# Kernel tuning notes

Hardware: AMD Instinct MI355X
Metric: run time of the kernel (lower is better)

## Reference

```python
import jax, jax.numpy as jnp
import numpy as np

HEAD_COUNT = 8  # matches init_kwargs head_count

def _branch(q_in, k_in, v_in, Wq, bq, Wk, bk, Wv, bv):
    # q_in/k_in/v_in: [B, N, D]. Linear (efficient) attention, per-head.
    B, N, D = q_in.shape
    H = HEAD_COUNT
    hd = D // H
    q = q_in @ Wq + bq            # [B, N, D]
    k = k_in @ Wk + bk
    v = v_in @ Wv + bv
    # permute(0,2,1) then contiguous channel slices per head == [B,H,hd,N]
    q = q.reshape(B, N, H, hd).transpose(0, 2, 3, 1)  # [B,H,hd,Nq]
    k = k.reshape(B, N, H, hd).transpose(0, 2, 3, 1)  # [B,H,hd,Nk]
    v = v.reshape(B, N, H, hd).transpose(0, 2, 3, 1)  # [B,H,hd,Nk]
    q = jax.nn.softmax(q, axis=3)  # softmax over sequence positions (torch dim=2)
    k = jax.nn.softmax(k, axis=2)  # softmax over head channels (torch dim=1)
    # context = k @ v^T : [B,H,hd_c,hd_d]
    ctx = jnp.einsum('bhcn,bhdn->bhcd', k, v)
    # attended = context^T @ q : [B,H,hd_d,Nq]
    att = jnp.einsum('bhcd,bhcn->bhdn', ctx, q)
    # concat heads along channel dim, then transpose -> [B, Nq, D]
    return att.reshape(B, D, N).transpose(0, 2, 1)

def setup_inputs() -> dict:
    key = jax.random.key(0)
    ks = jax.random.split(key, 16)
    B, N, D = 4, 8192, 256
    s = 0.02
    inp = {
        'f1': jax.random.normal(ks[0], (B, N, D), jnp.float32),
        'f2': jax.random.normal(ks[1], (B, N, D), jnp.float32),
        'f3': jax.random.normal(ks[2], (B, N, D), jnp.float32),
        'f4': jax.random.normal(ks[3], (B, N, D), jnp.float32),
        'f1_pos_embed': jax.random.normal(ks[4], (B, N, D), jnp.float32),
        'f2_pos_embed': jax.random.normal(ks[5], (B, N, D), jnp.float32),
        'f3_pos_embed': jax.random.normal(ks[6], (B, N, D), jnp.float32),
        'f4_pos_embed': jax.random.normal(ks[7], (B, N, D), jnp.float32),
        'Wq': jax.random.normal(ks[8], (3, D, D), jnp.float32) * s,
        'bq': jax.random.normal(ks[9], (3, D), jnp.float32) * s,
        'Wk': jax.random.normal(ks[10], (3, D, D), jnp.float32) * s,
        'bk': jax.random.normal(ks[11], (3, D), jnp.float32) * s,
        'Wv': jax.random.normal(ks[12], (3, D, D), jnp.float32) * s,
        'bv': jax.random.normal(ks[13], (3, D), jnp.float32) * s,
        'Wrp': jax.random.normal(ks[14], (3 * D, D), jnp.float32) * s,
        'brp': jax.random.normal(ks[15], (D,), jnp.float32) * s,
    }
    return inp

def reference(f1, f2, f3, f4, f1_pos_embed, f2_pos_embed, f3_pos_embed, f4_pos_embed,
              Wq, bq, Wk, bk, Wv, bv, Wrp, brp):
    q_in = f1 + f1_pos_embed
    agg21 = _branch(q_in, f2 + f2_pos_embed, f2, Wq[0], bq[0], Wk[0], bk[0], Wv[0], bv[0])
    agg31 = _branch(q_in, f3 + f3_pos_embed, f3, Wq[1], bq[1], Wk[1], bk[1], Wv[1], bv[1])
    agg41 = _branch(q_in, f4 + f4_pos_embed, f4, Wq[2], bq[2], Wk[2], bk[2], Wv[2], bv[2])
    out = jnp.concatenate([agg21, agg31, agg41], axis=-1)  # [B, N, 3D]
    return out @ Wrp + brp  # dropout p=0.0 -> identity
```

## Files before the change

kernel.cpp:

```cpp
#include <hip/hip_runtime.h>
#include <hip/hip_bf16.h>

typedef __attribute__((ext_vector_type(8))) short short8;
typedef __attribute__((ext_vector_type(4))) short shortx4;
typedef __attribute__((ext_vector_type(4))) float floatx4;
typedef __attribute__((ext_vector_type(16))) float floatx16;

#define N_SEQ 8192
#define M_ROWS 32768

__device__ __forceinline__ unsigned short f2bf(float f) {
    unsigned int x = __builtin_bit_cast(unsigned int, f);
    x += 0x7fff + ((x >> 16) & 1);
    return (unsigned short)(x >> 16);
}

__global__ __launch_bounds__(256) void transpose_w(
    const float* __restrict__ Wq, const float* __restrict__ Wk,
    const float* __restrict__ Wv, unsigned short* __restrict__ Wt)
{
    int job = blockIdx.x;
    int k = blockIdx.y;
    int n = threadIdx.x;
    const float* src =
        (job < 3) ? (Wq + job * 65536) :
        (job < 6) ? (Wk + (job - 3) * 65536) :
                    (Wv + (job - 6) * 65536);
    Wt[(size_t)job * 65536 + n * 256 + k] = f2bf(src[k * 256 + n]);
}

__global__ __launch_bounds__(256) void projq_kernel(
    const float* __restrict__ f1, const float* __restrict__ p1,
    const float* __restrict__ bq, const unsigned short* __restrict__ Wt,
    unsigned short* __restrict__ expQ, float* __restrict__ S)
{
    __shared__ __align__(16) unsigned short As[64][264];
    int m0 = blockIdx.x * 64;
    int b = m0 >> 13;
    int tid = threadIdx.x;
    int lane = tid & 63, wave = tid >> 6;
    int wm = wave >> 1, wn = wave & 1;
    int quad = lane >> 4, l15 = lane & 15;

    {
        int row = tid >> 2, seg = tid & 3;
        const float* fr = f1 + (size_t)(m0 + row) * 256 + seg * 64;
        const float* pr = p1 + (size_t)(m0 + row) * 256 + seg * 64;
        #pragma unroll
        for (int q = 0; q < 8; q++) {
            float4 x0 = *(const float4*)(fr + q * 8);
            float4 x1 = *(const float4*)(fr + q * 8 + 4);
            float4 y0 = *(const float4*)(pr + q * 8);
            float4 y1 = *(const float4*)(pr + q * 8 + 4);
            short8 v;
            v[0] = (short)f2bf(x0.x + y0.x); v[1] = (short)f2bf(x0.y + y0.y);
            v[2] = (short)f2bf(x0.z + y0.z); v[3] = (short)f2bf(x0.w + y0.w);
            v[4] = (short)f2bf(x1.x + y1.x); v[5] = (short)f2bf(x1.y + y1.y);
            v[6] = (short)f2bf(x1.z + y1.z); v[7] = (short)f2bf(x1.w + y1.w);
            *(short8*)&As[row][seg * 64 + q * 8] = v;
        }
    }
    __syncthreads();

    for (int nj = 0; nj < 6; nj++) {
        int j = nj >> 1;
        int n0 = (nj & 1) * 128;
        const unsigned short* Wj = Wt + (size_t)j * 65536;

        floatx4 acc[2][4];
        #pragma unroll
        for (int sm = 0; sm < 2; sm++)
            #pragma unroll
            for (int sn = 0; sn < 4; sn++)
                #pragma unroll
                for (int r = 0; r < 4; r++) acc[sm][sn][r] = 0.0f;

        #pragma unroll
        for (int ks = 0; ks < 8; ks++) {
            short8 af[2], bfr[4];
            #pragma unroll
            for (int sm = 0; sm < 2; sm++)
                af[sm] = *(const short8*)&As[wm * 32 + sm * 16 + l15][ks * 32 + quad * 8];
            #pragma unroll
            for (int sn = 0; sn < 4; sn++) {
                int ncol = n0 + wn * 64 + sn * 16 + l15;
                bfr[sn] = *(const short8*)(Wj + (size_t)ncol * 256 + ks * 32 + quad * 8);
            }
            #pragma unroll
            for (int sm = 0; sm < 2; sm++)
                #pragma unroll
                for (int sn = 0; sn < 4; sn++)
                    acc[sm][sn] = __builtin_amdgcn_mfma_f32_16x16x32_bf16(
                        af[sm], bfr[sn], acc[sm][sn], 0, 0, 0);
        }

        float colsum[4] = {0.f, 0.f, 0.f, 0.f};
        #pragma unroll
        for (int sm = 0; sm < 2; sm++)
            #pragma unroll
            for (int sn = 0; sn < 4; sn++) {
                float bb = bq[j * 256 + n0 + wn * 64 + sn * 16 + l15];
                #pragma unroll
                for (int r = 0; r < 4; r++) {
                    float e = __expf(acc[sm][sn][r] + bb);
                    colsum[sn] += e;
                    int row = m0 + wm * 32 + sm * 16 + quad * 4 + r;
                    int col = j * 256 + n0 + wn * 64 + sn * 16 + l15;
                    expQ[(size_t)row * 768 + col] = f2bf(e);
                }
            }
        #pragma unroll
        for (int sn = 0; sn < 4; sn++) {
            float v = colsum[sn];
            v += __shfl_xor(v, 16, 64);
            v += __shfl_xor(v, 32, 64);
            if (quad == 0)
                atomicAdd(&S[b * 768 + j * 256 + n0 + wn * 64 + sn * 16 + l15], v);
        }
    }
}

__global__ __launch_bounds__(512, 4) void projkv_ctx(
    const float* __restrict__ f2, const float* __restrict__ f3, const float* __restrict__ f4,
    const float* __restrict__ p2, const float* __restrict__ p3, const float* __restrict__ p4,
    const float* __restrict__ bk, const float* __restrict__ bv,
    const unsigned short* __restrict__ Wt, float* __restrict__ ctx)
{
    __shared__ __align__(16) unsigned short sh[36864];

    int tid = threadIdx.x;
    int lane = tid & 63, wn = tid >> 6;
    int quad = lane >> 4, l15 = lane & 15;
    int srow = tid >> 3, seg = tid & 7;

    int gbase = -1;
    int cur_ib = -1;
    const float *fin = nullptr, *pin = nullptr;
    const unsigned short *Wk_ = nullptr, *Wv_ = nullptr;
    float bkk[2] = {0.f, 0.f}, bvv[2] = {0.f, 0.f};
    floatx16 ctxacc;

    for (int j = 0; j < 3; j++) {
        int tau = blockIdx.x * 3 + j;
        int ib = tau >> 7;
        if (ib != cur_ib) {
            if (gbase >= 0) {
                int d = lane & 31;
                #pragma unroll
                for (int reg = 0; reg < 16; reg++) {
                    int cc = (reg & 3) + 8 * (reg >> 2) + 4 * (lane >> 5);
                    atomicAdd(&ctx[(size_t)gbase * 1024 + cc * 32 + d], ctxacc[reg]);
                }
            }
            cur_ib = ib;
            int b = ib & 3, i = ib >> 2;
            fin = ((i == 0) ? f2 : (i == 1) ? f3 : f4) + (size_t)b * N_SEQ * 256;
            pin = ((i == 0) ? p2 : (i == 1) ? p3 : p4) + (size_t)b * N_SEQ * 256;
            Wk_ = Wt + (size_t)(3 + i) * 65536;
            Wv_ = Wt + (size_t)(6 + i) * 65536;
            #pragma unroll
            for (int sn = 0; sn < 2; sn++) {
                bkk[sn] = bk[i * 256 + wn * 32 + sn * 16 + l15];
                bvv[sn] = bv[i * 256 + wn * 32 + sn * 16 + l15];
            }
            gbase = i * 32 + b * 8 + wn;
            #pragma unroll
            for (int q = 0; q < 16; q++) ctxacc[q] = 0.0f;
        }
        int m0 = (tau & 127) * 64;

        __syncthreads();
        {
            const float* fr = fin + (size_t)(m0 + srow) * 256;
            const float* pr = pin + (size_t)(m0 + srow) * 256;
            #pragma unroll
            for (int q = 0; q < 4; q++) {
                int c0 = q * 64 + seg * 8;
                float4 x0 = *(const float4*)(fr + c0);
                float4 x1 = *(const float4*)(fr + c0 + 4);
                float4 y0 = *(const float4*)(pr + c0);
                float4 y1 = *(const float4*)(pr + c0 + 4);
                short8 vv, kk;
                vv[0] = (short)f2bf(x0.x); kk[0] = (short)f2bf(x0.x + y0.x);
                vv[1] = (short)f2bf(x0.y); kk[1] = (short)f2bf(x0.y + y0.y);
                vv[2] = (short)f2bf(x0.z); kk[2] = (short)f2bf(x0.z + y0.z);
                vv[3] = (short)f2bf(x0.w); kk[3] = (short)f2bf(x0.w + y0.w);
                vv[4] = (short)f2bf(x1.x); kk[4] = (short)f2bf(x1.x + y1.x);
                vv[5] = (short)f2bf(x1.y); kk[5] = (short)f2bf(x1.y + y1.y);
                vv[6] = (short)f2bf(x1.z); kk[6] = (short)f2bf(x1.z + y1.z);
                vv[7] = (short)f2bf(x1.w); kk[7] = (short)f2bf(x1.w + y1.w);
                *(short8*)&sh[srow * 264 + c0] = kk;
                *(short8*)&sh[18432 + srow * 264 + c0] = vv;
            }
        }
        __syncthreads();

        floatx4 acc[4][2];
        #pragma unroll
        for (int sm = 0; sm < 4; sm++)
            #pragma unroll
            for (int sn = 0; sn < 2; sn++)
                #pragma unroll
                for (int r = 0; r < 4; r++) acc[sm][sn][r] = 0.0f;
        #pragma unroll
        for (int ks = 0; ks < 8; ks++) {
            short8 af[4], bfr[2];
            #pragma unroll
            for (int sm = 0; sm < 4; sm++)
                af[sm] = *(const short8*)&sh[(sm * 16 + l15) * 264 + ks * 32 + quad * 8];
            #pragma unroll
            for (int sn = 0; sn < 2; sn++) {
                int ncol = wn * 32 + sn * 16 + l15;
                bfr[sn] = *(const short8*)(Wk_ + (size_t)ncol * 256 + ks * 32 + quad * 8);
            }
            #pragma unroll
            for (int sm = 0; sm < 4; sm++)
                #pragma unroll
                for (int sn = 0; sn < 2; sn++)
                    acc[sm][sn] = __builtin_amdgcn_mfma_f32_16x16x32_bf16(
                        af[sm], bfr[sn], acc[sm][sn], 0, 0, 0);
        }
        #pragma unroll
        for (int sm = 0; sm < 4; sm++)
            #pragma unroll
            for (int r = 0; r < 4; r++) {
                float e0 = __expf(acc[sm][0][r] + bkk[0]);
                float e1 = __expf(acc[sm][1][r] + bkk[1]);
                float t = e0 + e1;
                t += __shfl_xor(t, 1, 64);
                t += __shfl_xor(t, 2, 64);
                t += __shfl_xor(t, 4, 64);
                t += __shfl_xor(t, 8, 64);
                float inv = 1.0f / t;
                acc[sm][0][r] = e0 * inv;
                acc[sm][1][r] = e1 * inv;
            }
        __syncthreads();
        #pragma unroll
        for (int sm = 0; sm < 4; sm++)
            #pragma unroll
            for (int sn = 0; sn < 2; sn++) {
                shortx4 v;
                #pragma unroll
                for (int r = 0; r < 4; r++) v[r] = (short)f2bf(acc[sm][sn][r]);
                *(shortx4*)&sh[(wn * 32 + sn * 16 + l15) * 72 + sm * 16 + quad * 4] = v;
            }

        #pragma unroll
        for (int sm = 0; sm < 4; sm++)
            #pragma unroll
            for (int sn = 0; sn < 2; sn++)
                #pragma unroll
                for (int r = 0; r < 4; r++) acc[sm][sn][r] = 0.0f;
        #pragma unroll
        for (int ks = 0; ks < 8; ks++) {
            short8 af[4], bfr[2];
            #pragma unroll
            for (int sm = 0; sm < 4; sm++)
                af[sm] = *(const short8*)&sh[18432 + (sm * 16 + l15) * 264 + ks * 32 + quad * 8];
            #pragma unroll
            for (int sn = 0; sn < 2; sn++) {
                int ncol = wn * 32 + sn * 16 + l15;
                bfr[sn] = *(const short8*)(Wv_ + (size_t)ncol * 256 + ks * 32 + quad * 8);
            }
            #pragma unroll
            for (int sm = 0; sm < 4; sm++)
                #pragma unroll
                for (int sn = 0; sn < 2; sn++)
                    acc[sm][sn] = __builtin_amdgcn_mfma_f32_16x16x32_bf16(
                        af[sm], bfr[sn], acc[sm][sn], 0, 0, 0);
        }
        __syncthreads();
        #pragma unroll
        for (int sm = 0; sm < 4; sm++)
            #pragma unroll
            for (int sn = 0; sn < 2; sn++) {
                shortx4 v;
                #pragma unroll
                for (int r = 0; r < 4; r++) v[r] = (short)f2bf(acc[sm][sn][r] + bvv[sn]);
                *(shortx4*)&sh[18432 + (wn * 32 + sn * 16 + l15) * 72 + sm * 16 + quad * 4] = v;
            }

        {
            int hc = wn * 32 + (lane & 31);
            int nb = (lane >> 5) * 8;
            #pragma unroll
            for (int s = 0; s < 4; s++) {
                short8 afr  = *(const short8*)&sh[hc * 72 + s * 16 + nb];
                short8 bfr2 = *(const short8*)&sh[18432 + hc * 72 + s * 16 + nb];
                ctxacc = __builtin_amdgcn_mfma_f32_32x32x16_bf16(afr, bfr2, ctxacc, 0, 0, 0);
            }
        }
    }

    if (gbase >= 0) {
        int d = lane & 31;
        #pragma unroll
        for (int reg = 0; reg < 16; reg++) {
            int cc = (reg & 3) + 8 * (reg >> 2) + 4 * (lane >> 5);
            atomicAdd(&ctx[(size_t)gbase * 1024 + cc * 32 + d], ctxacc[reg]);
        }
    }
}

__global__ __launch_bounds__(256) void wtilde_kernel(
    const float* __restrict__ ctx, const float* __restrict__ S,
    const float* __restrict__ Wrp, unsigned short* __restrict__ Wtld)
{
    __shared__ float cp[1024];
    int g = blockIdx.x;
    int i = g >> 5, b = (g >> 3) & 3, h = g & 7;
    int t = threadIdx.x;
    #pragma unroll
    for (int q = 0; q < 4; q++) {
        int idx = t + q * 256;
        int c = idx >> 5;
        cp[idx] = ctx[(size_t)g * 1024 + idx] / S[b * 768 + i * 256 + h * 32 + c];
    }
    __syncthreads();
    float accv[32];
    #pragma unroll
    for (int c = 0; c < 32; c++) accv[c] = 0.0f;
    for (int d = 0; d < 32; d++) {
        float w = Wrp[(size_t)(i * 256 + h * 32 + d) * 256 + t];
        #pragma unroll
        for (int c = 0; c < 32; c++) accv[c] += cp[c * 32 + d] * w;
    }
    for (int c = 0; c < 32; c++)
        Wtld[((size_t)b * 256 + t) * 768 + i * 256 + h * 32 + c] = f2bf(accv[c]);
}

__global__ __launch_bounds__(256) void out_kernel(
    const unsigned short* __restrict__ expQ, const unsigned short* __restrict__ Wtld,
    const float* __restrict__ brp, float* __restrict__ outp)
{
    __shared__ __align__(16) unsigned short As[128][72];
    int m0 = blockIdx.x * 128;
    int n0 = blockIdx.y * 128;
    int b = m0 >> 13;
    const unsigned short* Wb = Wtld + (size_t)b * 256 * 768;
    int tid = threadIdx.x;
    int lane = tid & 63, wave = tid >> 6;
    int wm = wave >> 1, wn = wave & 1;
    int quad = lane >> 4, l15 = lane & 15;

    floatx4 acc[4][4];
    #pragma unroll
    for (int a = 0; a < 4; a++)
        #pragma unroll
        for (int cc = 0; cc < 4; cc++)
            #pragma unroll
            for (int r = 0; r < 4; r++) acc[a][cc][r] = 0.0f;

    for (int kt = 0; kt < 12; kt++) {
        __syncthreads();
        #pragma unroll
        for (int p = 0; p < 4; p++) {
            int r = (tid >> 3) + p * 32;
            int kc = (tid & 7) * 8;
            size_t ga = (size_t)(m0 + r) * 768 + kt * 64 + kc;
            *(short8*)&As[r][kc] = *(const short8*)(expQ + ga);
        }
        __syncthreads();
        #pragma unroll
        for (int kc = 0; kc < 64; kc += 32) {
            short8 af[4], bfr[4];
            #pragma unroll
            for (int sm = 0; sm < 4; sm++)
                af[sm] = *(const short8*)&As[wm * 64 + sm * 16 + l15][kc + quad * 8];
            #pragma unroll
            for (int sn = 0; sn < 4; sn++) {
                int ncol = n0 + wn * 64 + sn * 16 + l15;
                bfr[sn] = *(const short8*)(Wb + (size_t)ncol * 768 + kt * 64 + kc + quad * 8);
            }
            #pragma unroll
            for (int sm = 0; sm < 4; sm++)
                #pragma unroll
                for (int sn = 0; sn < 4; sn++)
                    acc[sm][sn] = __builtin_amdgcn_mfma_f32_16x16x32_bf16(
                        af[sm], bfr[sn], acc[sm][sn], 0, 0, 0);
        }
    }

    float bb[4];
    #pragma unroll
    for (int sn = 0; sn < 4; sn++) bb[sn] = brp[n0 + wn * 64 + sn * 16 + l15];
    #pragma unroll
    for (int sm = 0; sm < 4; sm++)
        #pragma unroll
        for (int sn = 0; sn < 4; sn++)
            #pragma unroll
            for (int r = 0; r < 4; r++) {
                int row = m0 + wm * 64 + sm * 16 + quad * 4 + r;
                int col = n0 + wn * 64 + sn * 16 + l15;
                outp[(size_t)row * 256 + col] = acc[sm][sn][r] + bb[sn];
            }
}

extern "C" void kernel_launch(void* const* d_in, const int* in_sizes, int n_in,
                              void* d_out, int out_size, void* d_ws, size_t ws_size,
                              hipStream_t stream)
{
    (void)in_sizes; (void)n_in; (void)out_size; (void)ws_size;
    const float* f1  = (const float*)d_in[0];
    const float* f2  = (const float*)d_in[1];
    const float* f3  = (const float*)d_in[2];
    const float* f4  = (const float*)d_in[3];
    const float* p1  = (const float*)d_in[4];
    const float* p2  = (const float*)d_in[5];
    const float* p3  = (const float*)d_in[6];
    const float* p4  = (const float*)d_in[7];
    const float* Wq  = (const float*)d_in[8];
    const float* bq  = (const float*)d_in[9];
    const float* Wk  = (const float*)d_in[10];
    const float* bk  = (const float*)d_in[11];
    const float* Wv  = (const float*)d_in[12];
    const float* bv  = (const float*)d_in[13];
    const float* Wrp = (const float*)d_in[14];
    const float* brp = (const float*)d_in[15];

    char* ws = (char*)d_ws;
    unsigned short* expQ = (unsigned short*)(ws);
    unsigned short* Wt   = (unsigned short*)(ws + 50331648);
    unsigned short* Wtld = (unsigned short*)(ws + 51511296);
    float*          ctx  = (float*)(ws + 53084160);
    float*          S    = (float*)(ws + 53477376);

    hipMemsetAsync(ctx, 0, 393216 + 12288, stream);

    transpose_w<<<dim3(9, 256), 256, 0, stream>>>(Wq, Wk, Wv, Wt);
    projq_kernel<<<dim3(512), 256, 0, stream>>>(f1, p1, bq, Wt, expQ, S);
    projkv_ctx<<<dim3(512), 512, 0, stream>>>(f2, f3, f4, p2, p3, p4, bk, bv, Wt, ctx);
    wtilde_kernel<<<dim3(96), 256, 0, stream>>>(ctx, S, Wrp, Wtld);
    out_kernel<<<dim3(256, 2), 256, 0, stream>>>(expQ, Wtld, brp, (float*)d_out);
}
```

Measured before the change: 429.7 us.

## Prefetch next KV tile into registers and tile weight transpose through LDS

In projkv_ctx, the global loads of the next 64-row f/pos tile are issued into 16 float4 registers before the ctx MFMA stage, so memory latency overlaps with compute. This adds register pressure under launch_bounds(512,4) and could cause spills or lower occupancy. Separately, transpose_w now uses 64x64 LDS tiles with vectorized reads and writes instead of one scattered strided store per thread, launching 144 blocks instead of 2304.

```diff
diff --git a/kernel.cpp b/kernel.cpp
--- a/kernel.cpp
+++ b/kernel.cpp
@@ -19,14 +19,43 @@
     const float* __restrict__ Wq, const float* __restrict__ Wk,
     const float* __restrict__ Wv, unsigned short* __restrict__ Wt)
 {
+    __shared__ unsigned short tile[64][72];
     int job = blockIdx.x;
-    int k = blockIdx.y;
-    int n = threadIdx.x;
+    int tt = blockIdx.y;
+    int k0 = (tt >> 2) * 64, n0 = (tt & 3) * 64;
     const float* src =
         (job < 3) ? (Wq + job * 65536) :
         (job < 6) ? (Wk + (job - 3) * 65536) :
                     (Wv + (job - 6) * 65536);
-    Wt[(size_t)job * 65536 + n * 256 + k] = f2bf(src[k * 256 + n]);
+    int tid = threadIdx.x;
+    {
+        int r = tid >> 2, cs = (tid & 3) * 16;
+        const float* s = src + (size_t)(k0 + r) * 256 + n0 + cs;
+        #pragma unroll
+        for (int h = 0; h < 2; h++) {
+            float4 x0 = *(const float4*)(s + h * 8);
+            float4 x1 = *(const float4*)(s + h * 8 + 4);
+            short8 v;
+            v[0] = (short)f2bf(x0.x); v[1] = (short)f2bf(x0.y);
+            v[2] = (short)f2bf(x0.z); v[3] = (short)f2bf(x0.w);
+            v[4] = (short)f2bf(x1.x); v[5] = (short)f2bf(x1.y);
+            v[6] = (short)f2bf(x1.z); v[7] = (short)f2bf(x1.w);
+            *(short8*)&tile[r][cs + h * 8] = v;
+        }
+    }
+    __syncthreads();
+    {
+        int rn = tid >> 2, ks = (tid & 3) * 16;
+        unsigned short tmp[16];
+        #pragma unroll
+        for (int q = 0; q < 16; q++) tmp[q] = tile[ks + q][rn];
+        short8 v0, v1;
+        #pragma unroll
+        for (int q = 0; q < 8; q++) { v0[q] = (short)tmp[q]; v1[q] = (short)tmp[q + 8]; }
+        unsigned short* dst = Wt + (size_t)job * 65536 + (size_t)(n0 + rn) * 256 + k0 + ks;
+        *(short8*)dst = v0;
+        *(short8*)(dst + 8) = v1;
+    }
 }
 
 __global__ __launch_bounds__(256) void projq_kernel(
@@ -120,6 +149,28 @@
     }
 }
 
+__device__ __forceinline__ void pf_issue(
+    int tau, int srow, int seg,
+    const float* f2, const float* f3, const float* f4,
+    const float* p2, const float* p3, const float* p4,
+    float4 (&pf)[16])
+{
+    int ib = tau >> 7;
+    int b = ib & 3, i = ib >> 2;
+    const float* fb = ((i == 0) ? f2 : (i == 1) ? f3 : f4) + (size_t)b * N_SEQ * 256;
+    const float* pb = ((i == 0) ? p2 : (i == 1) ? p3 : p4) + (size_t)b * N_SEQ * 256;
+    const float* fr = fb + (size_t)((tau & 127) * 64 + srow) * 256;
+    const float* pr = pb + (size_t)((tau & 127) * 64 + srow) * 256;
+    #pragma unroll
+    for (int q = 0; q < 4; q++) {
+        int c0 = q * 64 + seg * 8;
+        pf[q * 4 + 0] = *(const float4*)(fr + c0);
+        pf[q * 4 + 1] = *(const float4*)(fr + c0 + 4);
+        pf[q * 4 + 2] = *(const float4*)(pr + c0);
+        pf[q * 4 + 3] = *(const float4*)(pr + c0 + 4);
+    }
+}
+
 __global__ __launch_bounds__(512, 4) void projkv_ctx(
     const float* __restrict__ f2, const float* __restrict__ f3, const float* __restrict__ f4,
     const float* __restrict__ p2, const float* __restrict__ p3, const float* __restrict__ p4,
@@ -135,10 +186,12 @@
 
     int gbase = -1;
     int cur_ib = -1;
-    const float *fin = nullptr, *pin = nullptr;
     const unsigned short *Wk_ = nullptr, *Wv_ = nullptr;
     float bkk[2] = {0.f, 0.f}, bvv[2] = {0.f, 0.f};
     floatx16 ctxacc;
+    float4 pf[16];
+
+    pf_issue(blockIdx.x * 3, srow, seg, f2, f3, f4, p2, p3, p4, pf);
 
     for (int j = 0; j < 3; j++) {
         int tau = blockIdx.x * 3 + j;
@@ -154,8 +207,6 @@
             }
             cur_ib = ib;
             int b = ib & 3, i = ib >> 2;
-            fin = ((i == 0) ? f2 : (i == 1) ? f3 : f4) + (size_t)b * N_SEQ * 256;
-            pin = ((i == 0) ? p2 : (i == 1) ? p3 : p4) + (size_t)b * N_SEQ * 256;
             Wk_ = Wt + (size_t)(3 + i) * 65536;
             Wv_ = Wt + (size_t)(6 + i) * 65536;
             #pragma unroll
@@ -167,19 +218,16 @@
             #pragma unroll
             for (int q = 0; q < 16; q++) ctxacc[q] = 0.0f;
         }
-        int m0 = (tau & 127) * 64;
 
         __syncthreads();
         {
-            const float* fr = fin + (size_t)(m0 + srow) * 256;
-            const float* pr = pin + (size_t)(m0 + srow) * 256;
             #pragma unroll
             for (int q = 0; q < 4; q++) {
                 int c0 = q * 64 + seg * 8;
-                float4 x0 = *(const float4*)(fr + c0);
-                float4 x1 = *(const float4*)(fr + c0 + 4);
-                float4 y0 = *(const float4*)(pr + c0);
-                float4 y1 = *(const float4*)(pr + c0 + 4);
+                float4 x0 = pf[q * 4 + 0];
+                float4 x1 = pf[q * 4 + 1];
+                float4 y0 = pf[q * 4 + 2];
+                float4 y1 = pf[q * 4 + 3];
                 short8 vv, kk;
                 vv[0] = (short)f2bf(x0.x); kk[0] = (short)f2bf(x0.x + y0.x);
                 vv[1] = (short)f2bf(x0.y); kk[1] = (short)f2bf(x0.y + y0.y);
@@ -280,6 +328,9 @@
                 for (int r = 0; r < 4; r++) v[r] = (short)f2bf(acc[sm][sn][r] + bvv[sn]);
                 *(shortx4*)&sh[18432 + (wn * 32 + sn * 16 + l15) * 72 + sm * 16 + quad * 4] = v;
             }
+
+        if (j < 2)
+            pf_issue(tau + 1, srow, seg, f2, f3, f4, p2, p3, p4, pf);
 
         {
             int hc = wn * 32 + (lane & 31);
@@ -428,7 +479,7 @@
 
     hipMemsetAsync(ctx, 0, 393216 + 12288, stream);
 
-    transpose_w<<<dim3(9, 256), 256, 0, stream>>>(Wq, Wk, Wv, Wt);
+    transpose_w<<<dim3(9, 16), 256, 0, stream>>>(Wq, Wk, Wv, Wt);
     projq_kernel<<<dim3(512), 256, 0, stream>>>(f1, p1, bq, Wt, expQ, S);
     projkv_ctx<<<dim3(512), 512, 0, stream>>>(f2, f3, f4, p2, p3, p4, bk, bv, Wt, ctx);
     wtilde_kernel<<<dim3(96), 256, 0, stream>>>(ctx, S, Wrp, Wtld);
```

After: 465.4 us. +8.3%, slower.

## Tile weight transpose, split projq columns across blocks, shrink out_kernel tiles

Applied to the files above, without the earlier changes.

Rewrites the weight transpose as a 64x64 shared-memory tiled transpose with vectorized loads and stores. It also splits the Q projection so two blocks each handle half of the output column chunks for the same row tile. The output GEMM tile shrinks to 64 rows, and both GEMM kernels get an occupancy hint so more blocks run concurrently on the device. The cost is that the projq split makes each row tile's f1/pos input be read and converted twice, and smaller output tiles reduce reuse of the B operand.

```diff
diff --git a/kernel.cpp b/kernel.cpp
--- a/kernel.cpp
+++ b/kernel.cpp
@@ -19,23 +19,53 @@
     const float* __restrict__ Wq, const float* __restrict__ Wk,
     const float* __restrict__ Wv, unsigned short* __restrict__ Wt)
 {
+    __shared__ unsigned short tile[64][72];
     int job = blockIdx.x;
-    int k = blockIdx.y;
-    int n = threadIdx.x;
+    int tt = blockIdx.y;
+    int k0 = (tt >> 2) * 64, n0 = (tt & 3) * 64;
     const float* src =
         (job < 3) ? (Wq + job * 65536) :
         (job < 6) ? (Wk + (job - 3) * 65536) :
                     (Wv + (job - 6) * 65536);
-    Wt[(size_t)job * 65536 + n * 256 + k] = f2bf(src[k * 256 + n]);
-}
-
-__global__ __launch_bounds__(256) void projq_kernel(
+    int tid = threadIdx.x;
+    {
+        int r = tid >> 2, cs = (tid & 3) * 16;
+        const float* s = src + (size_t)(k0 + r) * 256 + n0 + cs;
+        #pragma unroll
+        for (int h = 0; h < 2; h++) {
+            float4 x0 = *(const float4*)(s + h * 8);
+            float4 x1 = *(const float4*)(s + h * 8 + 4);
+            short8 v;
+            v[0] = (short)f2bf(x0.x); v[1] = (short)f2bf(x0.y);
+            v[2] = (short)f2bf(x0.z); v[3] = (short)f2bf(x0.w);
+            v[4] = (short)f2bf(x1.x); v[5] = (short)f2bf(x1.y);
+            v[6] = (short)f2bf(x1.z); v[7] = (short)f2bf(x1.w);
+            *(short8*)&tile[r][cs + h * 8] = v;
+        }
+    }
+    __syncthreads();
+    {
+        int rn = tid >> 2, ks = (tid & 3) * 16;
+        unsigned short tmp[16];
+        #pragma unroll
+        for (int q = 0; q < 16; q++) tmp[q] = tile[ks + q][rn];
+        short8 v0, v1;
+        #pragma unroll
+        for (int q = 0; q < 8; q++) { v0[q] = (short)tmp[q]; v1[q] = (short)tmp[q + 8]; }
+        unsigned short* dst = Wt + (size_t)job * 65536 + (size_t)(n0 + rn) * 256 + k0 + ks;
+        *(short8*)dst = v0;
+        *(short8*)(dst + 8) = v1;
+    }
+}
+
+__global__ __launch_bounds__(256, 4) void projq_kernel(
     const float* __restrict__ f1, const float* __restrict__ p1,
     const float* __restrict__ bq, const unsigned short* __restrict__ Wt,
     unsigned short* __restrict__ expQ, float* __restrict__ S)
 {
     __shared__ __align__(16) unsigned short As[64][264];
-    int m0 = blockIdx.x * 64;
+    int m0 = (blockIdx.x >> 1) * 64;
+    int ch = blockIdx.x & 1;
     int b = m0 >> 13;
     int tid = threadIdx.x;
     int lane = tid & 63, wave = tid >> 6;
@@ -62,9 +92,10 @@
     }
     __syncthreads();
 
-    for (int nj = 0; nj < 6; nj++) {
-        int j = nj >> 1;
-        int n0 = (nj & 1) * 128;
+    for (int njl = 0; njl < 3; njl++) {
+        int gnj = ch * 3 + njl;
+        int j = gnj >> 1;
+        int n0 = (gnj & 1) * 128;
         const unsigned short* Wj = Wt + (size_t)j * 65536;
 
         floatx4 acc[2][4];
@@ -330,51 +361,50 @@
         Wtld[((size_t)b * 256 + t) * 768 + i * 256 + h * 32 + c] = f2bf(accv[c]);
 }
 
-__global__ __launch_bounds__(256) void out_kernel(
+__global__ __launch_bounds__(256, 4) void out_kernel(
     const unsigned short* __restrict__ expQ, const unsigned short* __restrict__ Wtld,
     const float* __restrict__ brp, float* __restrict__ outp)
 {
-    __shared__ __align__(16) unsigned short As[128][72];
-    int m0 = blockIdx.x * 128;
-    int n0 = blockIdx.y * 128;
+    __shared__ __align__(16) unsigned short As[64][72];
+    int m0 = (blockIdx.x >> 1) * 64;
+    int n0 = (blockIdx.x & 1) * 128;
     int b = m0 >> 13;
     const unsigned short* Wb = Wtld + (size_t)b * 256 * 768;
     int tid = threadIdx.x;
     int lane = tid & 63, wave = tid >> 6;
     int wm = wave >> 1, wn = wave & 1;
     int quad = lane >> 4, l15 = lane & 15;
-
-    floatx4 acc[4][4];
+    int srow = tid >> 2, kc0 = (tid & 3) * 16;
+
+    floatx4 acc[2][4];
     #pragma unroll
-    for (int a = 0; a < 4; a++)
-        #pragma unroll
-        for (int cc = 0; cc < 4; cc++)
-            #pragma unroll
-            for (int r = 0; r < 4; r++) acc[a][cc][r] = 0.0f;
+    for (int sm = 0; sm < 2; sm++)
+        #pragma unroll
+        for (int sn = 0; sn < 4; sn++)
+            #pragma unroll
+            for (int r = 0; r < 4; r++) acc[sm][sn][r] = 0.0f;
 
     for (int kt = 0; kt < 12; kt++) {
         __syncthreads();
-        #pragma unroll
-        for (int p = 0; p < 4; p++) {
-            int r = (tid >> 3) + p * 32;
-            int kc = (tid & 7) * 8;
-            size_t ga = (size_t)(m0 + r) * 768 + kt * 64 + kc;
-            *(short8*)&As[r][kc] = *(const short8*)(expQ + ga);
+        {
+            size_t ga = (size_t)(m0 + srow) * 768 + kt * 64 + kc0;
+            *(short8*)&As[srow][kc0]     = *(const short8*)(expQ + ga);
+            *(short8*)&As[srow][kc0 + 8] = *(const short8*)(expQ + ga + 8);
         }
         __syncthreads();
         #pragma unroll
         for (int kc = 0; kc < 64; kc += 32) {
-            short8 af[4], bfr[4];
-            #pragma unroll
-            for (int sm = 0; sm < 4; sm++)
-                af[sm] = *(const short8*)&As[wm * 64 + sm * 16 + l15][kc + quad * 8];
+            short8 af[2], bfr[4];
+            #pragma unroll
+            for (int sm = 0; sm < 2; sm++)
+                af[sm] = *(const short8*)&As[wm * 32 + sm * 16 + l15][kc + quad * 8];
             #pragma unroll
             for (int sn = 0; sn < 4; sn++) {
                 int ncol = n0 + wn * 64 + sn * 16 + l15;
                 bfr[sn] = *(const short8*)(Wb + (size_t)ncol * 768 + kt * 64 + kc + quad * 8);
             }
             #pragma unroll
-            for (int sm = 0; sm < 4; sm++)
+            for (int sm = 0; sm < 2; sm++)
                 #pragma unroll
                 for (int sn = 0; sn < 4; sn++)
                     acc[sm][sn] = __builtin_amdgcn_mfma_f32_16x16x32_bf16(
@@ -386,12 +416,12 @@
     #pragma unroll
     for (int sn = 0; sn < 4; sn++) bb[sn] = brp[n0 + wn * 64 + sn * 16 + l15];
     #pragma unroll
-    for (int sm = 0; sm < 4; sm++)
+    for (int sm = 0; sm < 2; sm++)
         #pragma unroll
         for (int sn = 0; sn < 4; sn++)
             #pragma unroll
             for (int r = 0; r < 4; r++) {
-                int row = m0 + wm * 64 + sm * 16 + quad * 4 + r;
+                int row = m0 + wm * 32 + sm * 16 + quad * 4 + r;
                 int col = n0 + wn * 64 + sn * 16 + l15;
                 outp[(size_t)row * 256 + col] = acc[sm][sn][r] + bb[sn];
             }
@@ -428,9 +458,9 @@
 
     hipMemsetAsync(ctx, 0, 393216 + 12288, stream);
 
-    transpose_w<<<dim3(9, 256), 256, 0, stream>>>(Wq, Wk, Wv, Wt);
-    projq_kernel<<<dim3(512), 256, 0, stream>>>(f1, p1, bq, Wt, expQ, S);
+    transpose_w<<<dim3(9, 16), 256, 0, stream>>>(Wq, Wk, Wv, Wt);
+    projq_kernel<<<dim3(1024), 256, 0, stream>>>(f1, p1, bq, Wt, expQ, S);
     projkv_ctx<<<dim3(512), 512, 0, stream>>>(f2, f3, f4, p2, p3, p4, bk, bv, Wt, ctx);
     wtilde_kernel<<<dim3(96), 256, 0, stream>>>(ctx, S, Wrp, Wtld);
-    out_kernel<<<dim3(256, 2), 256, 0, stream>>>(expQ, Wtld, brp, (float*)d_out);
-}
+    out_kernel<<<dim3(1024), 256, 0, stream>>>(expQ, Wtld, brp, (float*)d_out);
+}
```

After: 473.9 us. +10.3%, slower.
